# Kernel optimization log

Measured on AMD Instinct MI355X. Metric: run time of the kernel, lower is better.

## Reference

```python
import jax, jax.numpy as jnp
import numpy as np

N = 100000
E = 1600000
IN = 128
HEADS = 8
HID = 16  # out_channels // heads
NEG_SLOPE = 0.2


def setup_inputs() -> dict:
    key = jax.random.key(0)
    k1, k2, k3, k4, k5 = jax.random.split(key, 5)
    x = jax.random.normal(k1, (N, IN), dtype=jnp.float32)
    edge_index = jax.random.randint(k2, (2, E), 0, N, dtype=jnp.int32)
    pos = jax.random.uniform(k3, (N,), dtype=jnp.float32)  # positive per-node weights
    W = jax.random.normal(k4, (HEADS * HID, IN), dtype=jnp.float32) * 0.1  # lin.weight
    att = jax.random.normal(k5, (1, HEADS, 2 * HID), dtype=jnp.float32) * 0.1
    return {"x": x, "edge_index": edge_index, "pos": pos, "W": W, "att": att}


def reference(x, edge_index, pos, W, att):
    n = x.shape[0]
    hid = att.shape[-1] // 2
    heads = att.shape[1]
    # linear projection: [N, heads, hid]
    h = (x @ W.T).reshape(n, heads, hid)
    row, col = edge_index[0], edge_index[1]
    # cat([h[row], h[col]], -1) * att -> sum(-1) == h[row].att_l + h[col].att_r
    att_l = att[0, :, :hid]   # [heads, hid]
    att_r = att[0, :, hid:]   # [heads, hid]
    al = jnp.einsum('nhd,hd->nh', h, att_l)  # [N, heads]
    ar = jnp.einsum('nhd,hd->nh', h, att_r)
    alpha = al[row] + ar[col]                # [E, heads]
    alpha = jnp.where(alpha >= 0, alpha, NEG_SLOPE * alpha)  # LeakyReLU
    # softmax_weights: exp, scale by pos[col], normalize by scatter row-sum
    alpha = jnp.exp(alpha) * pos[col][:, None]
    rowsum = jax.ops.segment_sum(alpha, row, num_segments=n)  # [N, heads]
    inv = 1.0 / rowsum + 1e-16
    alpha = alpha * inv[row]
    # weighted scatter-add aggregation
    out = jax.ops.segment_sum(alpha[:, :, None] * h[col], row, num_segments=n)
    return out.reshape(n, heads * hid)  # concat=True
```

## Files before the change

kernel.cpp:

```cpp
#include <hip/hip_runtime.h>
#include <hip/hip_fp16.h>


#define BK    256
#define BSH   8
#define NBMAX 512
#define BCAP  4736
#define EPB   8
#define GT    1024

typedef _Float16 half8 __attribute__((ext_vector_type(8)));
typedef float    f32x4 __attribute__((ext_vector_type(4)));

__global__ __launch_bounds__(256) void prep_w(
        const float* __restrict__ W, const float* __restrict__ att,
        _Float16* __restrict__ WBh, _Float16* __restrict__ WBl,
        int* __restrict__ gcur) {
    const int t = threadIdx.x;
    if (blockIdx.x == 0)
        for (int i = t; i < NBMAX; i += 256) gcur[i] = 0;
    int i = blockIdx.x * 256 + t;
    if (i >= 4 * 9 * 64 * 8) return;
    const int j    = i & 7;
    const int lane = (i >> 3) & 63;
    const int ctks = i >> 9;
    const int ct   = ctks % 9;
    const int ks   = ctks / 9;
    const int nn   = lane & 15;
    const int kg   = lane >> 4;
    const int k    = ks * 32 + kg * 8 + j;
    float w;
    if (ct < 8) {
        w = W[(ct * 16 + nn) * 128 + k];
    } else {
        const int head = nn & 7;
        const int sel  = nn >> 3;
        float s = 0.f;
        for (int d = 0; d < 16; ++d)
            s += att[head * 32 + sel * 16 + d] * W[(head * 16 + d) * 128 + k];
        w = s;
    }
    const _Float16 hi = (_Float16)w;
    WBh[i] = hi;
    WBl[i] = (_Float16)(w - (float)hi);
}

__global__ __launch_bounds__(512) void phase1(
        const float* __restrict__ x, const _Float16* __restrict__ WBh,
        const _Float16* __restrict__ WBl,
        _Float16* __restrict__ h, float* __restrict__ al,
        _Float16* __restrict__ arh,
        const int* __restrict__ ei, int* __restrict__ gcur,
        int* __restrict__ bins, int n, int E, int nb, int beBlocks) {
    __shared__ int  cnt[NBMAX];
    __shared__ int  basep[NBMAX];
    __shared__ int  lstart[NBMAX];
    __shared__ int2 sorted[512 * EPB];
    const int t = threadIdx.x;

    if ((int)blockIdx.x < beBlocks) {
        const int blk  = blockIdx.x;
        const int base = blk * (512 * EPB);
        cnt[t] = 0;
        __syncthreads();

        int rr[EPB], off[EPB];
#pragma unroll
        for (int j = 0; j < EPB; ++j) {
            const int e = base + j * 512 + t;
            if (e < E) {
                rr[j]  = ei[e];
                off[j] = atomicAdd(&cnt[rr[j] >> BSH], 1);
            } else rr[j] = -1;
        }
        __syncthreads();
        const int v = cnt[t];
        lstart[t] = v;
        __syncthreads();
        for (int o = 1; o < 512; o <<= 1) {
            const int tmp = (t >= o) ? lstart[t - o] : 0;
            __syncthreads();
            lstart[t] += tmp;
            __syncthreads();
        }
        const int incl = lstart[t];
        __syncthreads();
        lstart[t] = incl - v;
        basep[t]  = (t < nb && v > 0) ? atomicAdd(&gcur[t], v) : 0;
        __syncthreads();

#pragma unroll
        for (int j = 0; j < EPB; ++j) {
            if (rr[j] >= 0) {
                const int e = base + j * 512 + t;
                const int b = rr[j] >> BSH;
                sorted[lstart[b] + off[j]] = make_int2(ei[E + e], rr[j]);
            }
        }
        __syncthreads();

        const int total = lstart[511] + cnt[511];
        for (int i = t; i < total; i += 512) {
            const int2 p = sorted[i];
            const int  b = p.y >> BSH;
            const int  q = basep[b] + i - lstart[b];
            if (q < BCAP)
                bins[(size_t)b * BCAP + q] = p.x | ((p.y & (BK - 1)) << 17);
        }
    } else {
        const int blk  = blockIdx.x - beBlocks;
        const int wv   = t >> 6;
        const int lane = t & 63;
        const int m    = lane & 15;
        const int kg   = lane >> 4;
        const int nodeA = blk * 128 + wv * 16 + m;
        const bool avalid = nodeA < n;

        f32x4 acc[9];
#pragma unroll
        for (int ct = 0; ct < 9; ++ct) acc[ct] = (f32x4)0.f;

        const half8* bh = (const half8*)WBh;
        const half8* bl = (const half8*)WBl;

#pragma unroll
        for (int ks = 0; ks < 4; ++ks) {
            float xv[8];
            if (avalid) {
                const float4* xp =
                    (const float4*)&x[(size_t)nodeA * 128 + ks * 32 + kg * 8];
                *(float4*)&xv[0] = xp[0];
                *(float4*)&xv[4] = xp[1];
            } else {
#pragma unroll
                for (int j = 0; j < 8; ++j) xv[j] = 0.f;
            }
            half8 axh, axl;
#pragma unroll
            for (int j = 0; j < 8; ++j) {
                const _Float16 hi = (_Float16)xv[j];
                axh[j] = hi;
                axl[j] = (_Float16)(xv[j] - (float)hi);
            }
#pragma unroll
            for (int ct = 0; ct < 9; ++ct) {
                const half8 bhv = bh[(ks * 9 + ct) * 64 + lane];
                const half8 blv = bl[(ks * 9 + ct) * 64 + lane];
                acc[ct] = __builtin_amdgcn_mfma_f32_16x16x32_f16(axl, bhv, acc[ct], 0, 0, 0);
                acc[ct] = __builtin_amdgcn_mfma_f32_16x16x32_f16(axh, blv, acc[ct], 0, 0, 0);
                acc[ct] = __builtin_amdgcn_mfma_f32_16x16x32_f16(axh, bhv, acc[ct], 0, 0, 0);
            }
        }

        const int nodeD0 = blk * 128 + wv * 16 + kg * 4;
#pragma unroll
        for (int r = 0; r < 4; ++r) {
            const int node = nodeD0 + r;
            if (node < n) {
#pragma unroll
                for (int ct = 0; ct < 8; ++ct)
                    h[(size_t)node * 128 + ct * 16 + m] = (_Float16)acc[ct][r];
                if (m < 8) al[node * 8 + m] = acc[8][r];
                else       arh[node * 8 + (m - 8)] = (_Float16)acc[8][r];
            }
        }
    }
}

__global__ __launch_bounds__(GT) void bucket_gather(
        const int* __restrict__ bins, const int* __restrict__ gcur,
        const float* __restrict__ al, const _Float16* __restrict__ arh,
        const float* __restrict__ pos, const _Float16* __restrict__ h,
        float* __restrict__ out, int n) {
    __shared__ int sh[BCAP];
    __shared__ int csrL[BCAP];
    __shared__ int rstart[BK], sc[BK], cur[BK];
    const int b = blockIdx.x, t = threadIdx.x;
    if (t < BK) rstart[t] = 0;
    __syncthreads();
    const int cnt = min(gcur[b], BCAP);
    const int* bp = bins + (size_t)b * BCAP;
    for (int i = t; i < cnt; i += GT) {
        const int v = bp[i];
        sh[i] = v;
        atomicAdd(&rstart[((unsigned)v) >> 17], 1);
    }
    __syncthreads();
    if (t < BK) sc[t] = rstart[t];
    __syncthreads();
    for (int o = 1; o < BK; o <<= 1) {
        int tmp = 0;
        if (t < BK && t >= o) tmp = sc[t - o];
        __syncthreads();
        if (t < BK) sc[t] += tmp;
        __syncthreads();
    }
    if (t < BK) {
        const int v  = rstart[t];
        const int s0 = sc[t] - v;
        rstart[t] = s0;
        cur[t]    = s0;
    }
    __syncthreads();
    for (int i = t; i < cnt; i += GT) {
        const int vv = sh[i];
        const int q  = atomicAdd(&cur[((unsigned)vv) >> 17], 1);
        csrL[q] = vv & 0x1FFFF;
    }
    __syncthreads();

    const int wv   = t >> 6;
    const int lane = t & 63;
    const int sl   = lane & 15;
    const int hd   = lane & 7;
    const int es   = lane >> 3;
    const int esA  = lane >> 4;
    const int src  = sl >> 1;
    for (int rr = wv; rr < BK; rr += 16) {
        const int r = b * BK + rr;
        if (r >= n) break;
        const int s = rstart[rr];
        const int e = cur[rr];
        if (s >= e) {
            if (lane < 16) {
                float4 z = make_float4(0.f, 0.f, 0.f, 0.f);
                *(float4*)&out[(size_t)r * 128 + sl * 8]     = z;
                *(float4*)&out[(size_t)r * 128 + sl * 8 + 4] = z;
            }
            continue;
        }
        const float al_h = al[r * 8 + hd];
        float acc[8];
#pragma unroll
        for (int i = 0; i < 8; ++i) acc[i] = 0.f;
        float rs = 0.f;
        for (int j = s; j < e; j += 8) {
            const int  j1 = j + es;
            const bool v1 = j1 < e;
            const int  c1 = csrL[v1 ? j1 : s];
            float av = 0.f;
            if (v1) {
                float a = al_h + (float)arh[(size_t)c1 * 8 + hd];
                a  = (a >= 0.f) ? a : 0.2f * a;
                av = __expf(a) * pos[c1];
                rs += av;
            }
            {
                const int  jA = j + esA;
                const int  cA = csrL[(jA < e) ? jA : s];
                const float alpha = __shfl(av, esA * 8 + src, 64);
                const half8 hv = *(const half8*)&h[(size_t)cA * 128 + sl * 8];
#pragma unroll
                for (int i = 0; i < 8; ++i)
                    acc[i] = fmaf(alpha, (float)hv[i], acc[i]);
            }
            {
                const int  jB = j + 4 + esA;
                const int  cB = csrL[(jB < e) ? jB : s];
                const float alpha = __shfl(av, 32 + esA * 8 + src, 64);
                const half8 hv = *(const half8*)&h[(size_t)cB * 128 + sl * 8];
#pragma unroll
                for (int i = 0; i < 8; ++i)
                    acc[i] = fmaf(alpha, (float)hv[i], acc[i]);
            }
        }
        rs += __shfl_xor(rs, 8, 64);
        rs += __shfl_xor(rs, 16, 64);
        rs += __shfl_xor(rs, 32, 64);
#pragma unroll
        for (int i = 0; i < 8; ++i) {
            acc[i] += __shfl_xor(acc[i], 16, 64);
            acc[i] += __shfl_xor(acc[i], 32, 64);
        }
        const float rsh = __shfl(rs, src, 64);
        const float scl = (rsh != 0.f) ? (1.f / rsh + 1e-16f) : 0.f;
        if (lane < 16) {
            float4 o0 = make_float4(acc[0] * scl, acc[1] * scl,
                                    acc[2] * scl, acc[3] * scl);
            float4 o1 = make_float4(acc[4] * scl, acc[5] * scl,
                                    acc[6] * scl, acc[7] * scl);
            *(float4*)&out[(size_t)r * 128 + sl * 8]     = o0;
            *(float4*)&out[(size_t)r * 128 + sl * 8 + 4] = o1;
        }
    }
}

extern "C" void kernel_launch(void* const* d_in, const int* in_sizes, int n_in,
                              void* d_out, int out_size, void* d_ws, size_t ws_size,
                              hipStream_t stream) {
    const float* x   = nullptr;
    const int*   ei  = nullptr;
    const float* pos = nullptr;
    const float* W   = nullptr;
    const float* att = nullptr;
    int E2 = 0;
    for (int i = 0; i < n_in; ++i) {
        int s = in_sizes[i];
        if      (s == out_size)        x   = (const float*)d_in[i];
        else if (s == out_size / 128)  pos = (const float*)d_in[i];
        else if (s == 16384)           W   = (const float*)d_in[i];
        else if (s == 256)             att = (const float*)d_in[i];
        else { ei = (const int*)d_in[i]; E2 = s; }
    }
    float* out = (float*)d_out;
    const int N_ = out_size / 128;
    const int E_ = E2 / 2;
    const int NB = (N_ + BK - 1) / BK;

    _Float16* h   = (_Float16*)d_ws;
    float*    al  = (float*)(h + (size_t)N_ * 128);
    _Float16* arh = (_Float16*)(al + (size_t)N_ * 8);
    _Float16* WBh = arh + (size_t)N_ * 8;
    _Float16* WBl = WBh + 18432;
    int* gcur     = (int*)(WBl + 18432);
    int* bins     = gcur + NBMAX;

    const int nhBlocks = (N_ + 127) / 128;
    const int beBlocks = (E_ + 512 * EPB - 1) / (512 * EPB);

    prep_w<<<72, 256, 0, stream>>>(W, att, WBh, WBl, gcur);
    phase1<<<nhBlocks + beBlocks, 512, 0, stream>>>(
        x, WBh, WBl, h, al, arh, ei, gcur, bins, N_, E_, NB, beBlocks);
    bucket_gather<<<NB, GT, 0, stream>>>(bins, gcur, al, arh, pos, h, out, N_);
}
```

Measured before the change: 233.3 us.

## Split bucket gather into quarter-bucket 256-thread blocks with software-prefetched loads

Each bucket of 256 destination rows is now handled by four 256-thread blocks, each covering 64 rows. Each block rescans the bucket's edge list and keeps only its own rows, building a smaller shared CSR. This is meant to cut per-block shared memory and improve occupancy and load balance. The edge loop also prefetches the next iteration's column indices, arh, pos and h vectors into registers so global-load latency overlaps with the FMAs. The trade-offs are reading the bucket list four times, higher register pressure, and a hard QCAP cap that could silently drop edges if a quarter overflows.

```diff
diff --git a/kernel.cpp b/kernel.cpp
--- a/kernel.cpp
+++ b/kernel.cpp
@@ -7,7 +7,7 @@
 #define NBMAX 512
 #define BCAP  4736
 #define EPB   8
-#define GT    1024
+#define QCAP  2048
 
 typedef _Float16 half8 __attribute__((ext_vector_type(8)));
 typedef float    f32x4 __attribute__((ext_vector_type(4)));
@@ -167,45 +167,49 @@
     }
 }
 
-__global__ __launch_bounds__(GT) void bucket_gather(
+__global__ __launch_bounds__(256, 8) void bucket_gather(
         const int* __restrict__ bins, const int* __restrict__ gcur,
         const float* __restrict__ al, const _Float16* __restrict__ arh,
         const float* __restrict__ pos, const _Float16* __restrict__ h,
         float* __restrict__ out, int n) {
-    __shared__ int sh[BCAP];
-    __shared__ int csrL[BCAP];
-    __shared__ int rstart[BK], sc[BK], cur[BK];
-    const int b = blockIdx.x, t = threadIdx.x;
-    if (t < BK) rstart[t] = 0;
+    __shared__ int csrL[QCAP];
+    __shared__ int rst[64], cur[64], sc[64];
+    const int bq = blockIdx.x;
+    const int b  = bq >> 2;
+    const int q  = bq & 3;
+    const int t  = threadIdx.x;
+
+    if (t < 64) sc[t] = 0;
     __syncthreads();
     const int cnt = min(gcur[b], BCAP);
     const int* bp = bins + (size_t)b * BCAP;
-    for (int i = t; i < cnt; i += GT) {
-        const int v = bp[i];
-        sh[i] = v;
-        atomicAdd(&rstart[((unsigned)v) >> 17], 1);
-    }
-    __syncthreads();
-    if (t < BK) sc[t] = rstart[t];
-    __syncthreads();
-    for (int o = 1; o < BK; o <<= 1) {
+    for (int i = t; i < cnt; i += 256) {
+        const int rl = ((unsigned)bp[i]) >> 17;
+        if ((rl >> 6) == q) atomicAdd(&sc[rl & 63], 1);
+    }
+    __syncthreads();
+    const int vcnt = (t < 64) ? sc[t] : 0;
+    __syncthreads();
+    for (int o = 1; o < 64; o <<= 1) {
         int tmp = 0;
-        if (t < BK && t >= o) tmp = sc[t - o];
-        __syncthreads();
-        if (t < BK) sc[t] += tmp;
-        __syncthreads();
-    }
-    if (t < BK) {
-        const int v  = rstart[t];
-        const int s0 = sc[t] - v;
-        rstart[t] = s0;
-        cur[t]    = s0;
-    }
-    __syncthreads();
-    for (int i = t; i < cnt; i += GT) {
-        const int vv = sh[i];
-        const int q  = atomicAdd(&cur[((unsigned)vv) >> 17], 1);
-        csrL[q] = vv & 0x1FFFF;
+        if (t < 64 && t >= o) tmp = sc[t - o];
+        __syncthreads();
+        if (t < 64) sc[t] += tmp;
+        __syncthreads();
+    }
+    if (t < 64) {
+        const int s0 = sc[t] - vcnt;
+        rst[t] = s0;
+        cur[t] = s0;
+    }
+    __syncthreads();
+    for (int i = t; i < cnt; i += 256) {
+        const int v  = bp[i];
+        const int rl = ((unsigned)v) >> 17;
+        if ((rl >> 6) == q) {
+            const int p = atomicAdd(&cur[rl & 63], 1);
+            if (p < QCAP) csrL[p] = v & 0x1FFFF;
+        }
     }
     __syncthreads();
 
@@ -216,11 +220,11 @@
     const int es   = lane >> 3;
     const int esA  = lane >> 4;
     const int src  = sl >> 1;
-    for (int rr = wv; rr < BK; rr += 16) {
-        const int r = b * BK + rr;
+    for (int rr = wv; rr < 64; rr += 4) {
+        const int r = b * BK + q * 64 + rr;
         if (r >= n) break;
-        const int s = rstart[rr];
-        const int e = cur[rr];
+        const int s = min(rst[rr], QCAP);
+        const int e = min(cur[rr], QCAP);
         if (s >= e) {
             if (lane < 16) {
                 float4 z = make_float4(0.f, 0.f, 0.f, 0.f);
@@ -234,35 +238,42 @@
 #pragma unroll
         for (int i = 0; i < 8; ++i) acc[i] = 0.f;
         float rs = 0.f;
+        int c1 = csrL[(s + es      < e) ? s + es      : s];
+        int cA = csrL[(s + esA     < e) ? s + esA     : s];
+        int cB = csrL[(s + 4 + esA < e) ? s + 4 + esA : s];
+        _Float16 arc = arh[(size_t)c1 * 8 + hd];
+        float    poc = pos[c1];
+        half8 hA = *(const half8*)&h[(size_t)cA * 128 + sl * 8];
+        half8 hB = *(const half8*)&h[(size_t)cB * 128 + sl * 8];
         for (int j = s; j < e; j += 8) {
-            const int  j1 = j + es;
-            const bool v1 = j1 < e;
-            const int  c1 = csrL[v1 ? j1 : s];
+            const int jn  = (j + 8 < e) ? j + 8 : j;
+            const int c1n = csrL[(jn + es      < e) ? jn + es      : s];
+            const int cAn = csrL[(jn + esA     < e) ? jn + esA     : s];
+            const int cBn = csrL[(jn + 4 + esA < e) ? jn + 4 + esA : s];
+            const _Float16 arn = arh[(size_t)c1n * 8 + hd];
+            const float    pon = pos[c1n];
+            const half8 hAn = *(const half8*)&h[(size_t)cAn * 128 + sl * 8];
+            const half8 hBn = *(const half8*)&h[(size_t)cBn * 128 + sl * 8];
             float av = 0.f;
-            if (v1) {
-                float a = al_h + (float)arh[(size_t)c1 * 8 + hd];
+            if (j + es < e) {
+                float a = al_h + (float)arc;
                 a  = (a >= 0.f) ? a : 0.2f * a;
-                av = __expf(a) * pos[c1];
+                av = __expf(a) * poc;
                 rs += av;
             }
             {
-                const int  jA = j + esA;
-                const int  cA = csrL[(jA < e) ? jA : s];
                 const float alpha = __shfl(av, esA * 8 + src, 64);
-                const half8 hv = *(const half8*)&h[(size_t)cA * 128 + sl * 8];
 #pragma unroll
                 for (int i = 0; i < 8; ++i)
-                    acc[i] = fmaf(alpha, (float)hv[i], acc[i]);
+                    acc[i] = fmaf(alpha, (float)hA[i], acc[i]);
             }
             {
-                const int  jB = j + 4 + esA;
-                const int  cB = csrL[(jB < e) ? jB : s];
                 const float alpha = __shfl(av, 32 + esA * 8 + src, 64);
-                const half8 hv = *(const half8*)&h[(size_t)cB * 128 + sl * 8];
 #pragma unroll
                 for (int i = 0; i < 8; ++i)
-                    acc[i] = fmaf(alpha, (float)hv[i], acc[i]);
-            }
+                    acc[i] = fmaf(alpha, (float)hB[i], acc[i]);
+            }
+            arc = arn; poc = pon; hA = hAn; hB = hBn;
         }
         rs += __shfl_xor(rs, 8, 64);
         rs += __shfl_xor(rs, 16, 64);
@@ -321,5 +332,6 @@
     prep_w<<<72, 256, 0, stream>>>(W, att, WBh, WBl, gcur);
     phase1<<<nhBlocks + beBlocks, 512, 0, stream>>>(
         x, WBh, WBl, h, al, arh, ei, gcur, bins, N_, E_, NB, beBlocks);
-    bucket_gather<<<NB, GT, 0, stream>>>(bins, gcur, al, arh, pos, h, out, N_);
+    bucket_gather<<<NB * 4, 256, 0, stream>>>(bins, gcur, al, arh, pos, h,
+                                              out, N_);
 }
```

Measured after the change: 243.3 us. 1.04x slower.
